# Performance work log

Measured on AMD Instinct MI355X. Metric: run time of the kernel, lower is better.

Reference implementation:

```python
import jax, jax.numpy as jnp
import numpy as np

FREQ_THRESHOLD = 0.1


def setup_inputs() -> dict:
    key = jax.random.key(0)
    images = jax.random.uniform(key, (32, 3, 512, 512), dtype=jnp.float32)
    return {"images": images}


def reference(images):
    # images: [B, C, H, W]
    B, C, H, W = images.shape
    gray = jnp.mean(images, axis=1)                      # [B, H, W]
    fft_magnitude = jnp.abs(jnp.fft.fft2(gray))          # [B, H, W]

    # Radial low-frequency mask centered at (H//2, W//2) -- computed once,
    # shared across the batch (replaces the per-pixel Python loop).
    center_h, center_w = H // 2, W // 2
    radius = min(H, W) * FREQ_THRESHOLD
    yy = jnp.arange(H, dtype=jnp.float32)[:, None]
    xx = jnp.arange(W, dtype=jnp.float32)[None, :]
    dist = jnp.sqrt((yy - center_h) ** 2 + (xx - center_w) ** 2)
    low_freq_mask = (dist <= radius).astype(fft_magnitude.dtype)  # [H, W]

    low_freq_energy = jnp.sum(fft_magnitude * low_freq_mask, axis=(1, 2))  # [B]
    total_energy = jnp.sum(fft_magnitude, axis=(1, 2))                     # [B]
    mura_scores = low_freq_energy / total_energy                           # [B]
    return jnp.mean(mura_scores)                                           # scalar
```

## Files before the change

### kernel.cpp

```cpp
#include <hip/hip_runtime.h>
#include <math.h>

#define N 512
#define NPAD(i) ((i) + ((i) >> 5))
#define FSZ 532
#define NCOL 257
#define RAD2 2621.44f
#define SQ2H 0.70710678f

__device__ __forceinline__ void dft8(float (&xr)[8], float (&xi)[8]) {
    float e0r = xr[0] + xr[4], e0i = xi[0] + xi[4];
    float e1r = xr[0] - xr[4], e1i = xi[0] - xi[4];
    float e2r = xr[2] + xr[6], e2i = xi[2] + xi[6];
    float e3r = xr[2] - xr[6], e3i = xi[2] - xi[6];
    float E0r = e0r + e2r, E0i = e0i + e2i;
    float E2r = e0r - e2r, E2i = e0i - e2i;
    float E1r = e1r + e3i, E1i = e1i - e3r;
    float E3r = e1r - e3i, E3i = e1i + e3r;
    float o0r = xr[1] + xr[5], o0i = xi[1] + xi[5];
    float o1r = xr[1] - xr[5], o1i = xi[1] - xi[5];
    float o2r = xr[3] + xr[7], o2i = xi[3] + xi[7];
    float o3r = xr[3] - xr[7], o3i = xi[3] - xi[7];
    float O0r = o0r + o2r, O0i = o0i + o2i;
    float O2r = o0r - o2r, O2i = o0i - o2i;
    float O1r = o1r + o3i, O1i = o1i - o3r;
    float O3r = o1r - o3i, O3i = o1i + o3r;
    float t1r = SQ2H * (O1r + O1i), t1i = SQ2H * (O1i - O1r);
    float t2r = O2i,                t2i = -O2r;
    float t3r = SQ2H * (O3i - O3r), t3i = -SQ2H * (O3r + O3i);
    xr[0] = E0r + O0r; xi[0] = E0i + O0i;
    xr[4] = E0r - O0r; xi[4] = E0i - O0i;
    xr[1] = E1r + t1r; xi[1] = E1i + t1i;
    xr[5] = E1r - t1r; xi[5] = E1i - t1i;
    xr[2] = E2r + t2r; xi[2] = E2i + t2i;
    xr[6] = E2r - t2r; xi[6] = E2i - t2i;
    xr[3] = E3r + t3r; xi[3] = E3i + t3i;
    xr[7] = E3r - t3r; xi[7] = E3i - t3i;
}

__device__ __forceinline__ void fft512_regs(float (&zr)[8], float (&zi)[8],
                                            int l) {
#pragma unroll
    for (int half = 32; half >= 1; half >>= 1) {
        const int j = l & (half - 1);
        const float f = (float)j * (0.5f / (float)half);
        const float c = __builtin_amdgcn_cosf(f);
        const float s = __builtin_amdgcn_sinf(f);
        const bool up = (l & half) != 0;
        const float sgn = up ? -1.0f : 1.0f;
        const float wc  = up ? c : 1.0f;
        const float ws  = up ? s : 0.0f;
#pragma unroll
        for (int k = 0; k < 8; ++k) {
            float pr = __shfl_xor(zr[k], half);
            float pi = __shfl_xor(zi[k], half);
            float tr = fmaf(sgn, zr[k], pr);
            float ti = fmaf(sgn, zi[k], pi);
            zr[k] = tr * wc + ti * ws;
            zi[k] = ti * wc - tr * ws;
        }
    }
    const int w = __brev((unsigned)l) >> 26;
#pragma unroll
    for (int k = 1; k < 8; ++k) {
        const float f = (float)(k * w) * (1.0f / 512.0f);
        const float c = __builtin_amdgcn_cosf(f);
        const float s = __builtin_amdgcn_sinf(f);
        float tr = zr[k] * c + zi[k] * s;
        float ti = zi[k] * c - zr[k] * s;
        zr[k] = tr; zi[k] = ti;
    }
    dft8(zr, zi);
}

__global__ __launch_bounds__(512) void k_gray_rowfft(
    const float* __restrict__ img, float2* __restrict__ buf) {
    __shared__ float sr[8][FSZ], si[8][FSZ];
    const int t = threadIdx.x, wv = t >> 6, l = t & 63;
    const int b = blockIdx.y, tile = blockIdx.x;
    const size_t plane = (size_t)N * N;
    const float* base = img + (size_t)b * 3 * plane;
    const int he = tile * 16 + 2 * wv;
    const float* p0 = base + (size_t)he * N;
    const float* p1 = p0 + N;

    const float4* c0e = (const float4*)(p0);
    const float4* c1e = (const float4*)(p0 + plane);
    const float4* c2e = (const float4*)(p0 + 2 * plane);
    const float4* c0o = (const float4*)(p1);
    const float4* c1o = (const float4*)(p1 + plane);
    const float4* c2o = (const float4*)(p1 + 2 * plane);

    float zr[8], zi[8];
    const float inv3 = 1.0f / 3.0f;
#pragma unroll
    for (int q = 0; q < 2; ++q) {
        int idx = 2 * l + q;
        float4 a = c0e[idx], bb = c1e[idx], c = c2e[idx];
        float4 d = c0o[idx], e = c1o[idx], g = c2o[idx];
        zr[4 * q + 0] = (a.x + bb.x + c.x) * inv3;
        zr[4 * q + 1] = (a.y + bb.y + c.y) * inv3;
        zr[4 * q + 2] = (a.z + bb.z + c.z) * inv3;
        zr[4 * q + 3] = (a.w + bb.w + c.w) * inv3;
        zi[4 * q + 0] = (d.x + e.x + g.x) * inv3;
        zi[4 * q + 1] = (d.y + e.y + g.y) * inv3;
        zi[4 * q + 2] = (d.z + e.z + g.z) * inv3;
        zi[4 * q + 3] = (d.w + e.w + g.w) * inv3;
    }

    fft512_regs(zr, zi, l);

    const int w = __brev((unsigned)l) >> 26;
#pragma unroll
    for (int k = 0; k < 8; ++k) {
        int u = w + 64 * k;
        sr[wv][NPAD(u)] = zr[k];
        si[wv][NPAD(u)] = zi[k];
    }
    __syncthreads();

    const int p = t & 7;
    const int h2 = 2 * p;
    const int slot = t >> 3;
    float2* ob = buf + (size_t)b * NCOL * N;
#pragma unroll
    for (int it = 0; it < 5; ++it) {
        int v = slot + 64 * it;
        if (v < NCOL) {
            int vn = (N - v) & (N - 1);
            float Zr  = sr[p][NPAD(v)],  Zi  = si[p][NPAD(v)];
            float Zr2 = sr[p][NPAD(vn)], Zi2 = si[p][NPAD(vn)];
            float4 o;
            o.x = 0.5f * (Zr + Zr2);
            o.y = 0.5f * (Zi - Zi2);
            o.z = 0.5f * (Zi + Zi2);
            o.w = 0.5f * (Zr2 - Zr);
            *(float4*)(&ob[(size_t)v * N + tile * 16 + h2]) = o;
        }
    }
}

__global__ __launch_bounds__(256) void k_colfft_reduce(
    const float2* __restrict__ buf, float* __restrict__ acc) {
    __shared__ float red[8];
    const int t = threadIdx.x, wv = t >> 6, l = t & 63;
    const int b = blockIdx.y;
    const int v = blockIdx.x * 4 + wv;
    const int vv = v > 256 ? 256 : v;

    const float4* col = (const float4*)(buf + ((size_t)b * NCOL + vv) * N);
    float zr[8], zi[8];
#pragma unroll
    for (int q = 0; q < 4; ++q) {
        float4 z = col[4 * l + q];
        zr[2 * q]     = z.x; zi[2 * q]     = z.y;
        zr[2 * q + 1] = z.z; zi[2 * q + 1] = z.w;
    }

    fft512_regs(zr, zi, l);

    const float wcol = (v == 0 || v == 256) ? 1.0f : (v < 256 ? 2.0f : 0.0f);
    const float dx = (float)(vv - 256);
    const float dx2 = dx * dx;
    const int w = __brev((unsigned)l) >> 26;
    float msum = 0.0f, tsum = 0.0f;
#pragma unroll
    for (int k = 0; k < 8; ++k) {
        int u = w + 64 * k;
        float mag = sqrtf(zr[k] * zr[k] + zi[k] * zi[k]);
        tsum += mag;
        float dy = (float)(u - 256);
        if (dy * dy + dx2 <= RAD2) msum += mag;
    }
    msum *= wcol; tsum *= wcol;
#pragma unroll
    for (int off = 32; off > 0; off >>= 1) {
        msum += __shfl_down(msum, off);
        tsum += __shfl_down(tsum, off);
    }
    if (l == 0) { red[wv * 2] = msum; red[wv * 2 + 1] = tsum; }
    __syncthreads();
    if (t == 0) {
        atomicAdd(&acc[b * 2 + 0], red[0] + red[2] + red[4] + red[6]);
        atomicAdd(&acc[b * 2 + 1], red[1] + red[3] + red[5] + red[7]);
    }
}

__global__ void k_final(const float* __restrict__ acc,
                        float* __restrict__ out) {
    int t = threadIdx.x;
    float r = 0.0f;
    if (t < 32) r = acc[t * 2 + 0] / acc[t * 2 + 1];
#pragma unroll
    for (int off = 32; off > 0; off >>= 1) r += __shfl_down(r, off);
    if (t == 0) out[0] = r * (1.0f / 32.0f);
}

extern "C" void kernel_launch(void* const* d_in, const int* in_sizes, int n_in,
                              void* d_out, int out_size, void* d_ws,
                              size_t ws_size, hipStream_t stream) {
    const float* img = (const float*)d_in[0];
    float* out = (float*)d_out;

    float2* buf = (float2*)d_ws;
    const size_t buf_bytes = (size_t)32 * NCOL * N * sizeof(float2);
    float* acc = (float*)((char*)d_ws + buf_bytes);

    hipMemsetAsync(acc, 0, 64 * sizeof(float), stream);

    dim3 g1(N / 16, 32);
    k_gray_rowfft<<<g1, 512, 0, stream>>>(img, buf);

    dim3 g2((NCOL + 3) / 4, 32);
    k_colfft_reduce<<<g2, 256, 0, stream>>>(buf, acc);

    k_final<<<1, 64, 0, stream>>>(acc, out);
}
```

Before: 185.7 us.

## Store intermediate row-FFT buffer in fp16 and fuse final reduction into column kernel

```diff
diff --git a/kernel.cpp b/kernel.cpp
--- a/kernel.cpp
+++ b/kernel.cpp
@@ -1,4 +1,5 @@
 #include <hip/hip_runtime.h>
+#include <hip/hip_fp16.h>
 #include <math.h>
 
 #define N 512
@@ -7,6 +8,7 @@
 #define NCOL 257
 #define RAD2 2621.44f
 #define SQ2H 0.70710678f
+#define K2_BLOCKS (65 * 32)
 
 __device__ __forceinline__ void dft8(float (&xr)[8], float (&xi)[8]) {
     float e0r = xr[0] + xr[4], e0i = xi[0] + xi[4];
@@ -74,7 +76,7 @@
 }
 
 __global__ __launch_bounds__(512) void k_gray_rowfft(
-    const float* __restrict__ img, float2* __restrict__ buf) {
+    const float* __restrict__ img, __half2* __restrict__ bufh) {
     __shared__ float sr[8][FSZ], si[8][FSZ];
     const int t = threadIdx.x, wv = t >> 6, l = t & 63;
     const int b = blockIdx.y, tile = blockIdx.x;
@@ -122,7 +124,7 @@
     const int p = t & 7;
     const int h2 = 2 * p;
     const int slot = t >> 3;
-    float2* ob = buf + (size_t)b * NCOL * N;
+    __half2* ob = bufh + (size_t)b * NCOL * N;
 #pragma unroll
     for (int it = 0; it < 5; ++it) {
         int v = slot + 64 * it;
@@ -130,31 +132,40 @@
             int vn = (N - v) & (N - 1);
             float Zr  = sr[p][NPAD(v)],  Zi  = si[p][NPAD(v)];
             float Zr2 = sr[p][NPAD(vn)], Zi2 = si[p][NPAD(vn)];
-            float4 o;
-            o.x = 0.5f * (Zr + Zr2);
-            o.y = 0.5f * (Zi - Zi2);
-            o.z = 0.5f * (Zi + Zi2);
-            o.w = 0.5f * (Zr2 - Zr);
-            *(float4*)(&ob[(size_t)v * N + tile * 16 + h2]) = o;
+            __half2 fe = __floats2half2_rn(0.5f * (Zr + Zr2),
+                                           0.5f * (Zi - Zi2));
+            __half2 fo = __floats2half2_rn(0.5f * (Zi + Zi2),
+                                           0.5f * (Zr2 - Zr));
+            __half2 pairv[2] = {fe, fo};
+            *(uint2*)(&ob[(size_t)v * N + tile * 16 + h2]) =
+                *(const uint2*)pairv;
         }
     }
 }
 
 __global__ __launch_bounds__(256) void k_colfft_reduce(
-    const float2* __restrict__ buf, float* __restrict__ acc) {
+    const __half2* __restrict__ bufh, float* __restrict__ acc,
+    unsigned* __restrict__ cnt, float* __restrict__ out) {
     __shared__ float red[8];
+    __shared__ int isLast;
     const int t = threadIdx.x, wv = t >> 6, l = t & 63;
     const int b = blockIdx.y;
     const int v = blockIdx.x * 4 + wv;
     const int vv = v > 256 ? 256 : v;
 
-    const float4* col = (const float4*)(buf + ((size_t)b * NCOL + vv) * N);
+    const uint4* col = (const uint4*)(bufh + ((size_t)b * NCOL + vv) * N);
     float zr[8], zi[8];
 #pragma unroll
-    for (int q = 0; q < 4; ++q) {
-        float4 z = col[4 * l + q];
-        zr[2 * q]     = z.x; zi[2 * q]     = z.y;
-        zr[2 * q + 1] = z.z; zi[2 * q + 1] = z.w;
+    for (int q = 0; q < 2; ++q) {
+        uint4 raw = col[2 * l + q];
+        float2 z0 = __half22float2(*(const __half2*)&raw.x);
+        float2 z1 = __half22float2(*(const __half2*)&raw.y);
+        float2 z2 = __half22float2(*(const __half2*)&raw.z);
+        float2 z3 = __half22float2(*(const __half2*)&raw.w);
+        zr[4 * q + 0] = z0.x; zi[4 * q + 0] = z0.y;
+        zr[4 * q + 1] = z1.x; zi[4 * q + 1] = z1.y;
+        zr[4 * q + 2] = z2.x; zi[4 * q + 2] = z2.y;
+        zr[4 * q + 3] = z3.x; zi[4 * q + 3] = z3.y;
     }
 
     fft512_regs(zr, zi, l);
@@ -183,17 +194,24 @@
     if (t == 0) {
         atomicAdd(&acc[b * 2 + 0], red[0] + red[2] + red[4] + red[6]);
         atomicAdd(&acc[b * 2 + 1], red[1] + red[3] + red[5] + red[7]);
-    }
-}
-
-__global__ void k_final(const float* __restrict__ acc,
-                        float* __restrict__ out) {
-    int t = threadIdx.x;
-    float r = 0.0f;
-    if (t < 32) r = acc[t * 2 + 0] / acc[t * 2 + 1];
-#pragma unroll
-    for (int off = 32; off > 0; off >>= 1) r += __shfl_down(r, off);
-    if (t == 0) out[0] = r * (1.0f / 32.0f);
+        __threadfence();
+        unsigned tick = atomicAdd(cnt, 1u);
+        isLast = (tick == (unsigned)(K2_BLOCKS - 1));
+    }
+    __syncthreads();
+    if (isLast) {
+        float r = 0.0f;
+        if (t < 32) {
+            float m = atomicAdd(&acc[t * 2 + 0], 0.0f);
+            float s = atomicAdd(&acc[t * 2 + 1], 0.0f);
+            r = m / s;
+        }
+        if (t < 64) {
+#pragma unroll
+            for (int off = 32; off > 0; off >>= 1) r += __shfl_down(r, off);
+            if (t == 0) out[0] = r * (1.0f / 32.0f);
+        }
+    }
 }
 
 extern "C" void kernel_launch(void* const* d_in, const int* in_sizes, int n_in,
@@ -202,17 +220,16 @@
     const float* img = (const float*)d_in[0];
     float* out = (float*)d_out;
 
-    float2* buf = (float2*)d_ws;
-    const size_t buf_bytes = (size_t)32 * NCOL * N * sizeof(float2);
+    __half2* bufh = (__half2*)d_ws;
+    const size_t buf_bytes = (size_t)32 * NCOL * N * sizeof(__half2);
     float* acc = (float*)((char*)d_ws + buf_bytes);
-
-    hipMemsetAsync(acc, 0, 64 * sizeof(float), stream);
+    unsigned* cnt = (unsigned*)(acc + 64);
+
+    hipMemsetAsync(acc, 0, 65 * sizeof(float), stream);
 
     dim3 g1(N / 16, 32);
-    k_gray_rowfft<<<g1, 512, 0, stream>>>(img, buf);
+    k_gray_rowfft<<<g1, 512, 0, stream>>>(img, bufh);
 
     dim3 g2((NCOL + 3) / 4, 32);
-    k_colfft_reduce<<<g2, 256, 0, stream>>>(buf, acc);
-
-    k_final<<<1, 64, 0, stream>>>(acc, out);
-}
+    k_colfft_reduce<<<g2, 256, 0, stream>>>(bufh, acc, cnt, out);
+}
```

After: 199.7 us. 1.08x slower.
